# Optimization experiments

Hardware: AMD Instinct MI355X
Metric: run time of the kernel (lower is better)

Reference implementation:

```python
import jax, jax.numpy as jnp
import numpy as np

B, S, N1, N2, NS = 2048, 1024, 8192, 16384, 256
EPS = 1e-10

def setup_inputs() -> dict:
    key = jax.random.key(0)
    ks = jax.random.split(key, 12)
    t_in = jax.random.uniform(ks[0], (B,), jnp.float32)
    y_in = jax.random.uniform(ks[1], (B, S), jnp.float32)
    den_gas = jax.random.uniform(ks[2], (B, 1), jnp.float32) * 1e4
    alpha_1st = jax.random.uniform(ks[3], (N1,), jnp.float32)
    gamma_1st = jax.random.uniform(ks[4], (N1,), jnp.float32) * 50.0
    alpha_2nd = jax.random.uniform(ks[5], (N2,), jnp.float32)
    gamma_2nd = jax.random.uniform(ks[6], (N2,), jnp.float32) * 50.0
    r1_1st = jax.random.randint(ks[7], (N1,), 0, S, jnp.int32)
    p_1st = jax.random.randint(ks[8], (N1,), 0, S, jnp.int32)
    r1_2nd = jax.random.randint(ks[9], (N2,), 0, S, jnp.int32)
    r2_2nd = jax.random.randint(ks[10], (N2,), 0, S, jnp.int32)
    p_2nd = jax.random.randint(ks[11], (N2,), 0, S, jnp.int32)
    inds_surf = 512 + jnp.arange(NS, dtype=jnp.int32)  # surface species slots
    inds_mant = 768 + jnp.arange(NS, dtype=jnp.int32)  # mantle species slots
    return dict(t_in=t_in, y_in=y_in, den_gas=den_gas,
                alpha_1st=alpha_1st, gamma_1st=gamma_1st,
                alpha_2nd=alpha_2nd, gamma_2nd=gamma_2nd,
                r1_1st=r1_1st, p_1st=p_1st,
                r1_2nd=r1_2nd, r2_2nd=r2_2nd, p_2nd=p_2nd,
                inds_surf=inds_surf, inds_mant=inds_mant)

def reference(t_in, y_in, den_gas, alpha_1st, gamma_1st, alpha_2nd, gamma_2nd,
              r1_1st, p_1st, r1_2nd, r2_2nd, p_2nd, inds_surf, inds_mant):
    zeros = jnp.zeros_like(y_in)
    # medium parameters (module_med): temperature from t, den_norm from den_gas
    T = 10.0 + 5.0 * jax.nn.sigmoid(t_in)[:, None]            # [B,1]
    # rmod_1st / rmod_2nd: modified-Arrhenius rate coefficients
    rates_1st = alpha_1st[None, :] * jnp.exp(-gamma_1st[None, :] / T)      # [B,N1]
    rates_2nd = (alpha_2nd[None, :] * jnp.sqrt(T / 300.0)
                 * jnp.exp(-gamma_2nd[None, :] / T))                       # [B,N2]
    # reaction fluxes (gather)
    terms_1st = rates_1st * y_in[:, r1_1st]                                 # [B,N1]
    terms_2nd = rates_2nd * y_in[:, r1_2nd] * y_in[:, r2_2nd] * den_gas     # [B,N2]
    # surface gain / loss assemblers (gain-only and loss-only scatters)
    gain = (zeros.at[:, p_1st].add(terms_1st)
                 .at[:, p_2nd].add(terms_2nd))[:, inds_surf]
    loss = (zeros.at[:, r1_1st].add(-terms_1st)
                 .at[:, r1_2nd].add(-terms_2nd)
                 .at[:, r2_2nd].add(-terms_2nd))[:, inds_surf]
    dy_surf_gain = jnp.sum(gain, axis=-1, keepdims=True)    # [B,1] >= 0
    dy_surf_loss = -jnp.sum(loss, axis=-1, keepdims=True)   # [B,1] >= 0
    # rmod_smt: surface<->mantle transfer coefficients (three-phase)
    y_surf_tot = jnp.sum(y_in[:, inds_surf], axis=-1, keepdims=True)
    y_mant_tot = jnp.sum(y_in[:, inds_mant], axis=-1, keepdims=True)
    k_s2m = dy_surf_gain / (y_surf_tot + EPS)  # burial rate per surface species
    k_m2s = dy_surf_loss / (y_mant_tot + EPS)  # excavation rate per mantle species
    terms_s2m = k_s2m * y_in[:, inds_surf]     # [B,NS]
    terms_m2s = k_m2s * y_in[:, inds_mant]     # [B,NS]
    # full RHS: asm_smt + asm_1st + asm_2nd
    dy = (zeros
          .at[:, p_1st].add(terms_1st).at[:, r1_1st].add(-terms_1st)
          .at[:, p_2nd].add(terms_2nd)
          .at[:, r1_2nd].add(-terms_2nd).at[:, r2_2nd].add(-terms_2nd)
          .at[:, inds_surf].add(terms_m2s - terms_s2m)
          .at[:, inds_mant].add(terms_s2m - terms_m2s))
    return dy
```

## Files before the change

### kernel.cpp

```cpp
#include <hip/hip_runtime.h>
#include <hip/hip_fp16.h>

constexpr int kB  = 2048;
constexpr int kS  = 1024;
constexpr int kN1 = 8192;
constexpr int kN2 = 16384;
constexpr int kNTERM = kN1 + kN2;
constexpr int kQT    = kNTERM / 4;
constexpr int kRoles = 2*kN1 + 3*kN2;
constexpr float kEPS = 1e-10f;
constexpr int NT = 256;

constexpr int kGrpPitch[8] = {24, 24, 24, 32, 24, 40, 24, 40};
constexpr int kGrpBase [8] = {0, 24576, 49152, 73728, 106496, 131072, 172032, 196608};
constexpr int kEllWords    = 237568;
constexpr int kCurWords    = 8 * kS;

constexpr size_t kWsMid  = (size_t)(kCurWords + kEllWords) * 4;
constexpr size_t kWsFull = kWsMid + (size_t)kNTERM * 16;

__global__ __launch_bounds__(NT) void ell_fill(
    const float* __restrict__ a1, const float* __restrict__ g1,
    const float* __restrict__ a2, const float* __restrict__ g2,
    const int* __restrict__ r1_1, const int* __restrict__ p_1,
    const int* __restrict__ r1_2, const int* __restrict__ r2_2,
    const int* __restrict__ p_2,
    unsigned* __restrict__ cursor, unsigned* __restrict__ ell,
    float4* __restrict__ rec)
{
    int i = blockIdx.x * NT + threadIdx.x;
    if (i >= kRoles) return;
    int s, j; bool neg;
    if (i < kN1)                  { j = i;          s = p_1[j];  neg = false; }
    else if (i < 2*kN1)           { j = i - kN1;    s = r1_1[j]; neg = true;  }
    else if (i < 2*kN1 + kN2)     { int q = i - 2*kN1;         j = kN1 + q; s = p_2[q];  neg = false; }
    else if (i < 2*kN1 + 2*kN2)   { int q = i - 2*kN1 - kN2;   j = kN1 + q; s = r1_2[q]; neg = true; }
    else                          { int q = i - 2*kN1 - 2*kN2; j = kN1 + q; s = r2_2[q]; neg = true; }
    int qq = j / kQT;
    unsigned addr = (unsigned)(j - qq * kQT + 1) << 2;
    int grp = qq * 2 + (neg ? 1 : 0);
    unsigned k = atomicAdd(&cursor[grp * kS + s], 1u);
    if (k < (unsigned)kGrpPitch[grp])
        ell[(unsigned)kGrpBase[grp] + ((k >> 2) * kS + s) * 4 + (k & 3)] = addr;

    if (rec && i < kNTERM) {
        float4 r;
        if (i < kN1) { r.x = a1[i]; r.y = -g1[i]; r.z = __int_as_float(r1_1[i]); r.w = 0.f; }
        else { int q = i - kN1; r.x = a2[q]; r.y = -g2[q];
               r.z = __int_as_float(r1_2[q]); r.w = __int_as_float(r2_2[q]); }
        rec[i] = r;
    }
}

__device__ __forceinline__ void glist2(
    const uint4* __restrict__ bp, const uint4* __restrict__ bn, int s,
    int cp, int cn, const __half2* t2,
    float& p0, float& p1, float& n0, float& n1)
{
    int tp = (cp + 3) >> 2;
    int tn = (cn + 3) >> 2;
    int T  = tp > tn ? tp : tn;
    const uint4* ap = bp + s;
    const uint4* an = bn + s;
    for (int t = 0; t < T; ++t) {
        bool dp = t < tp, dn = t < tn;
        uint4 ep, en;
        if (dp) ep = *ap;
        if (dn) en = *an;
        ap += kS; an += kS;
        if (dp) {
            float2 f0 = __half22float2(*(const __half2*)((const char*)t2 + ep.x));
            float2 f1 = __half22float2(*(const __half2*)((const char*)t2 + ep.y));
            float2 f2 = __half22float2(*(const __half2*)((const char*)t2 + ep.z));
            float2 f3 = __half22float2(*(const __half2*)((const char*)t2 + ep.w));
            p0 += (f0.x + f1.x) + (f2.x + f3.x);
            p1 += (f0.y + f1.y) + (f2.y + f3.y);
        }
        if (dn) {
            float2 f0 = __half22float2(*(const __half2*)((const char*)t2 + en.x));
            float2 f1 = __half22float2(*(const __half2*)((const char*)t2 + en.y));
            float2 f2 = __half22float2(*(const __half2*)((const char*)t2 + en.z));
            float2 f3 = __half22float2(*(const __half2*)((const char*)t2 + en.w));
            n0 += (f0.x + f1.x) + (f2.x + f3.x);
            n1 += (f0.y + f1.y) + (f2.y + f3.y);
        }
    }
}

template<bool REC>
__global__ __launch_bounds__(NT, 4) void three_phase_gather4(
    const float* __restrict__ t_in, const float* __restrict__ y_in,
    const float* __restrict__ den_gas,
    const float* __restrict__ a1, const float* __restrict__ g1,
    const float* __restrict__ a2, const float* __restrict__ g2,
    const int* __restrict__ r1_1,
    const int* __restrict__ r1_2, const int* __restrict__ r2_2,
    const unsigned* __restrict__ cursor, const unsigned* __restrict__ ell,
    const float4* __restrict__ rec, float* __restrict__ dy)
{
    __shared__ float2  y2[kS];
    __shared__ __half2 terms2[kQT + 1];
    __shared__ float   red[4][8];

    const int tid = threadIdx.x;
    const int b0  = blockIdx.x * 2;

    {
        const float4* s0 = (const float4*)(y_in + (size_t)b0 * kS);
        const float4* s1 = (const float4*)(y_in + (size_t)(b0 + 1) * kS);
        float4 va = s0[tid], vb = s1[tid];
        y2[4*tid+0] = make_float2(va.x, vb.x);
        y2[4*tid+1] = make_float2(va.y, vb.y);
        y2[4*tid+2] = make_float2(va.z, vb.z);
        y2[4*tid+3] = make_float2(va.w, vb.w);
    }
    if (tid == 0) terms2[0] = __halves2half2(__float2half(0.f), __float2half(0.f));

    float T0 = 10.f + 5.f / (1.f + __expf(-t_in[b0]));
    float T1 = 10.f + 5.f / (1.f + __expf(-t_in[b0 + 1]));
    float i0 = 1.f / T0, i1 = 1.f / T1;
    float c20 = __fsqrt_rn(T0 * (1.f / 300.f)) * den_gas[b0];
    float c21 = __fsqrt_rn(T1 * (1.f / 300.f)) * den_gas[b0 + 1];

    float acc[4][2] = {};
    float gn[2] = {}, ls[2] = {};

    #pragma unroll
    for (int q = 0; q < 4; ++q) {
        __syncthreads();
        const int base = q * kQT;
        #pragma unroll 2
        for (int it = 0; it < kQT / NT; ++it) {
            int j = base + it * NT + tid;
            float al, ng; int ra, rb;
            if (REC) {
                float4 r = rec[j];
                al = r.x; ng = r.y;
                ra = __float_as_int(r.z); rb = __float_as_int(r.w);
            } else if (j < kN1) {
                al = a1[j]; ng = -g1[j]; ra = r1_1[j]; rb = 0;
            } else {
                int u = j - kN1;
                al = a2[u]; ng = -g2[u]; ra = r1_2[u]; rb = r2_2[u];
            }
            float t0, t1;
            if (j < kN1) {
                float2 ya = y2[ra];
                t0 = al * __expf(ng * i0) * ya.x;
                t1 = al * __expf(ng * i1) * ya.y;
            } else {
                float2 ya = y2[ra], yb = y2[rb];
                t0 = c20 * al * __expf(ng * i0) * ya.x * yb.x;
                t1 = c21 * al * __expf(ng * i1) * ya.y * yb.y;
            }
            terms2[j - base + 1] = __halves2half2(__float2half(t0), __float2half(t1));
        }
        __syncthreads();
        const unsigned* cp = cursor + (2*q)     * kS;
        const unsigned* cn = cursor + (2*q + 1) * kS;
        const uint4* bp = (const uint4*)(ell + kGrpBase[2*q]);
        const uint4* bn = (const uint4*)(ell + kGrpBase[2*q + 1]);
        #pragma unroll
        for (int slot = 0; slot < 4; ++slot) {
            int s = tid + slot * NT;
            int ccp = (int)cp[s]; ccp = ccp < kGrpPitch[2*q]   ? ccp : kGrpPitch[2*q];
            int ccn = (int)cn[s]; ccn = ccn < kGrpPitch[2*q+1] ? ccn : kGrpPitch[2*q+1];
            float p0 = 0.f, p1 = 0.f, n0 = 0.f, n1 = 0.f;
            glist2(bp, bn, s, ccp, ccn, terms2, p0, p1, n0, n1);
            acc[slot][0] += p0 - n0;
            acc[slot][1] += p1 - n1;
            if (slot == 2) { gn[0] += p0; gn[1] += p1; ls[0] += n0; ls[1] += n1; }
        }
    }

    float ys0 = y2[512 + tid].x, ys1 = y2[512 + tid].y;
    float ym0 = y2[768 + tid].x, ym1 = y2[768 + tid].y;
    float v[8] = {gn[0], ls[0], ys0, ym0, gn[1], ls[1], ys1, ym1};
    #pragma unroll
    for (int off = 32; off > 0; off >>= 1) {
        #pragma unroll
        for (int w = 0; w < 8; ++w) v[w] += __shfl_down(v[w], off, 64);
    }
    int wave = tid >> 6;
    if ((tid & 63) == 0) {
        #pragma unroll
        for (int w = 0; w < 8; ++w) red[wave][w] = v[w];
    }
    __syncthreads();
    float tv[8];
    #pragma unroll
    for (int w = 0; w < 8; ++w) tv[w] = red[0][w] + red[1][w] + red[2][w] + red[3][w];

    float ks2m0 = tv[0] / (tv[2] + kEPS), km2s0 = tv[1] / (tv[3] + kEPS);
    float ks2m1 = tv[4] / (tv[6] + kEPS), km2s1 = tv[5] / (tv[7] + kEPS);

    float* o0 = dy + (size_t)b0 * kS;
    float* o1 = o0 + kS;
    o0[tid]       = acc[0][0];
    o0[tid + 256] = acc[1][0];
    o0[tid + 512] = acc[2][0] + km2s0 * ym0 - ks2m0 * ys0;
    o0[tid + 768] = acc[3][0] + ks2m0 * ys0 - km2s0 * ym0;
    o1[tid]       = acc[0][1];
    o1[tid + 256] = acc[1][1];
    o1[tid + 512] = acc[2][1] + km2s1 * ym1 - ks2m1 * ys1;
    o1[tid + 768] = acc[3][1] + ks2m1 * ys1 - km2s1 * ym1;
}

__global__ __launch_bounds__(NT) void three_phase_scatter(
    const float* __restrict__ t_in, const float* __restrict__ y_in,
    const float* __restrict__ den_gas,
    const float* __restrict__ alpha_1st, const float* __restrict__ gamma_1st,
    const float* __restrict__ alpha_2nd, const float* __restrict__ gamma_2nd,
    const int* __restrict__ r1_1st, const int* __restrict__ p_1st,
    const int* __restrict__ r1_2nd, const int* __restrict__ r2_2nd,
    const int* __restrict__ p_2nd, float* __restrict__ dy)
{
    __shared__ float y_row[kS];
    __shared__ float accs[kS];
    __shared__ float tot[4];
    const int tid = threadIdx.x;
    const int b   = blockIdx.x;
    ((float4*)y_row)[tid] = ((const float4*)(y_in + (size_t)b * kS))[tid];
    ((float4*)accs)[tid] = make_float4(0.f, 0.f, 0.f, 0.f);
    if (tid < 4) tot[tid] = 0.f;
    float t = t_in[b];
    float T = 10.f + 5.f / (1.f + __expf(-t));
    float invT = 1.f / T, sqT = __fsqrt_rn(T * (1.f / 300.f)), dg = den_gas[b];
    __syncthreads();
    float gain = 0.f, loss = 0.f;
    for (int j = tid; j < kN1; j += NT) {
        int r1 = r1_1st[j], p = p_1st[j];
        float term = alpha_1st[j] * __expf(-gamma_1st[j] * invT) * y_row[r1];
        atomicAdd(&accs[p], term); atomicAdd(&accs[r1], -term);
        if ((unsigned)(p - 512) < 256u) gain += term;
        if ((unsigned)(r1 - 512) < 256u) loss += term;
    }
    for (int j = tid; j < kN2; j += NT) {
        int r1 = r1_2nd[j], r2 = r2_2nd[j], p = p_2nd[j];
        float term = sqT * dg * alpha_2nd[j] * __expf(-gamma_2nd[j] * invT) * y_row[r1] * y_row[r2];
        atomicAdd(&accs[p], term); atomicAdd(&accs[r1], -term); atomicAdd(&accs[r2], -term);
        if ((unsigned)(p - 512) < 256u) gain += term;
        if ((unsigned)(r1 - 512) < 256u) loss += term;
        if ((unsigned)(r2 - 512) < 256u) loss += term;
    }
    float g = gain, l = loss;
    #pragma unroll
    for (int off = 32; off > 0; off >>= 1) { g += __shfl_down(g, off, 64); l += __shfl_down(l, off, 64); }
    if ((tid & 63) == 0) { atomicAdd(&tot[0], g); atomicAdd(&tot[1], l); }
    __syncthreads();
    if (tid < 64) {
        float a2v = 0.f;
        for (int u = tid; u < 256; u += 64) a2v += y_row[512 + u];
        #pragma unroll
        for (int off = 32; off > 0; off >>= 1) a2v += __shfl_down(a2v, off, 64);
        if (tid == 0) tot[2] = a2v;
    } else if (tid < 128) {
        float m2 = 0.f;
        for (int u = tid - 64; u < 256; u += 64) m2 += y_row[768 + u];
        #pragma unroll
        for (int off = 32; off > 0; off >>= 1) m2 += __shfl_down(m2, off, 64);
        if (tid == 64) tot[3] = m2;
    }
    __syncthreads();
    float k_s2m = tot[0] / (tot[2] + kEPS);
    float k_m2s = tot[1] / (tot[3] + kEPS);
    float* out = dy + (size_t)b * kS;
    for (int s = tid; s < kS; s += NT) {
        float v = accs[s];
        if ((unsigned)(s - 512) < 256u) v += k_m2s * y_row[s + 256] - k_s2m * y_row[s];
        else if (s >= 768)              v += k_s2m * y_row[s - 256] - k_m2s * y_row[s];
        out[s] = v;
    }
}

extern "C" void kernel_launch(void* const* d_in, const int* in_sizes, int n_in,
                              void* d_out, int out_size, void* d_ws, size_t ws_size,
                              hipStream_t stream) {
    const float* t_in      = (const float*)d_in[0];
    const float* y_in      = (const float*)d_in[1];
    const float* den_gas   = (const float*)d_in[2];
    const float* alpha_1st = (const float*)d_in[3];
    const float* gamma_1st = (const float*)d_in[4];
    const float* alpha_2nd = (const float*)d_in[5];
    const float* gamma_2nd = (const float*)d_in[6];
    const int*   r1_1st    = (const int*)d_in[7];
    const int*   p_1st     = (const int*)d_in[8];
    const int*   r1_2nd    = (const int*)d_in[9];
    const int*   r2_2nd    = (const int*)d_in[10];
    const int*   p_2nd     = (const int*)d_in[11];
    float* dy = (float*)d_out;

    if (ws_size >= kWsMid) {
        unsigned* cursor = (unsigned*)d_ws;
        unsigned* ell    = cursor + kCurWords;
        float4*   rec    = (ws_size >= kWsFull)
                         ? (float4*)((char*)d_ws + kWsMid) : (float4*)nullptr;
        hipMemsetAsync(d_ws, 0, kWsMid, stream);
        ell_fill<<<kRoles / NT, NT, 0, stream>>>(
            alpha_1st, gamma_1st, alpha_2nd, gamma_2nd,
            r1_1st, p_1st, r1_2nd, r2_2nd, p_2nd, cursor, ell, rec);
        if (rec)
            three_phase_gather4<true><<<kB / 2, NT, 0, stream>>>(
                t_in, y_in, den_gas, alpha_1st, gamma_1st, alpha_2nd, gamma_2nd,
                r1_1st, r1_2nd, r2_2nd, cursor, ell, rec, dy);
        else
            three_phase_gather4<false><<<kB / 2, NT, 0, stream>>>(
                t_in, y_in, den_gas, alpha_1st, gamma_1st, alpha_2nd, gamma_2nd,
                r1_1st, r1_2nd, r2_2nd, cursor, ell, rec, dy);
    } else {
        three_phase_scatter<<<kB, NT, 0, stream>>>(
            t_in, y_in, den_gas, alpha_1st, gamma_1st, alpha_2nd, gamma_2nd,
            r1_1st, p_1st, r1_2nd, r2_2nd, p_2nd, dy);
    }
}
```

Before: 166.6 us.

## Pack ELL indices into 16-bit halves and prefetch first ELL row before barrier

```diff
diff --git a/kernel.cpp b/kernel.cpp
--- a/kernel.cpp
+++ b/kernel.cpp
@@ -11,10 +11,10 @@
 constexpr float kEPS = 1e-10f;
 constexpr int NT = 256;
 
-constexpr int kGrpPitch[8] = {24, 24, 24, 32, 24, 40, 24, 40};
-constexpr int kGrpBase [8] = {0, 24576, 49152, 73728, 106496, 131072, 172032, 196608};
-constexpr int kEllWords    = 237568;
-constexpr int kCurWords    = 8 * kS;
+constexpr int kGrpPitchE[8] = {24, 24, 24, 32, 24, 40, 24, 40};
+constexpr int kGrpBase [8]  = {0, 12288, 24576, 36864, 53248, 65536, 86016, 98304};
+constexpr int kEllWords     = 118784;
+constexpr int kCurWords     = 8 * kS;
 
 constexpr size_t kWsMid  = (size_t)(kCurWords + kEllWords) * 4;
 constexpr size_t kWsFull = kWsMid + (size_t)kNTERM * 16;
@@ -40,8 +40,11 @@
     unsigned addr = (unsigned)(j - qq * kQT + 1) << 2;
     int grp = qq * 2 + (neg ? 1 : 0);
     unsigned k = atomicAdd(&cursor[grp * kS + s], 1u);
-    if (k < (unsigned)kGrpPitch[grp])
-        ell[(unsigned)kGrpBase[grp] + ((k >> 2) * kS + s) * 4 + (k & 3)] = addr;
+    if (k < (unsigned)kGrpPitchE[grp]) {
+        unsigned w = (unsigned)kGrpBase[grp]
+                   + ((k >> 3) * (unsigned)kS + (unsigned)s) * 4u + ((k >> 1) & 3u);
+        atomicOr(&ell[w], addr << ((k & 1u) * 16u));
+    }
 
     if (rec && i < kNTERM) {
         float4 r;
@@ -52,43 +55,45 @@
     }
 }
 
-__device__ __forceinline__ void glist2(
-    const uint4* __restrict__ bp, const uint4* __restrict__ bn, int s,
-    int cp, int cn, const __half2* t2,
+__device__ __forceinline__ void accum8(uint4 e, const __half2* __restrict__ t2,
+                                       float& r0, float& r1)
+{
+    const char* tb = (const char*)t2;
+    float2 f0 = __half22float2(*(const __half2*)(tb + (e.x & 0xffffu)));
+    float2 f1 = __half22float2(*(const __half2*)(tb + (e.x >> 16)));
+    float2 f2 = __half22float2(*(const __half2*)(tb + (e.y & 0xffffu)));
+    float2 f3 = __half22float2(*(const __half2*)(tb + (e.y >> 16)));
+    float2 f4 = __half22float2(*(const __half2*)(tb + (e.z & 0xffffu)));
+    float2 f5 = __half22float2(*(const __half2*)(tb + (e.z >> 16)));
+    float2 f6 = __half22float2(*(const __half2*)(tb + (e.w & 0xffffu)));
+    float2 f7 = __half22float2(*(const __half2*)(tb + (e.w >> 16)));
+    r0 += ((f0.x + f1.x) + (f2.x + f3.x)) + ((f4.x + f5.x) + (f6.x + f7.x));
+    r1 += ((f0.y + f1.y) + (f2.y + f3.y)) + ((f4.y + f5.y) + (f6.y + f7.y));
+}
+
+__device__ __forceinline__ void glist2_pf(
+    const uint4* __restrict__ ap, const uint4* __restrict__ an,
+    uint4 ep, uint4 en, int cp, int cn, const __half2* __restrict__ t2,
     float& p0, float& p1, float& n0, float& n1)
 {
-    int tp = (cp + 3) >> 2;
-    int tn = (cn + 3) >> 2;
-    int T  = tp > tn ? tp : tn;
-    const uint4* ap = bp + s;
-    const uint4* an = bn + s;
-    for (int t = 0; t < T; ++t) {
+    accum8(ep, t2, p0, p1);
+    accum8(en, t2, n0, n1);
+    int tp = (cp + 7) >> 3;
+    int tn = (cn + 7) >> 3;
+    int T = tp > tn ? tp : tn;
+    for (int t = 1; t < T; ++t) {
         bool dp = t < tp, dn = t < tn;
-        uint4 ep, en;
-        if (dp) ep = *ap;
-        if (dn) en = *an;
+        uint4 e2, e3;
+        if (dp) e2 = *ap;
+        if (dn) e3 = *an;
         ap += kS; an += kS;
-        if (dp) {
-            float2 f0 = __half22float2(*(const __half2*)((const char*)t2 + ep.x));
-            float2 f1 = __half22float2(*(const __half2*)((const char*)t2 + ep.y));
-            float2 f2 = __half22float2(*(const __half2*)((const char*)t2 + ep.z));
-            float2 f3 = __half22float2(*(const __half2*)((const char*)t2 + ep.w));
-            p0 += (f0.x + f1.x) + (f2.x + f3.x);
-            p1 += (f0.y + f1.y) + (f2.y + f3.y);
-        }
-        if (dn) {
-            float2 f0 = __half22float2(*(const __half2*)((const char*)t2 + en.x));
-            float2 f1 = __half22float2(*(const __half2*)((const char*)t2 + en.y));
-            float2 f2 = __half22float2(*(const __half2*)((const char*)t2 + en.z));
-            float2 f3 = __half22float2(*(const __half2*)((const char*)t2 + en.w));
-            n0 += (f0.x + f1.x) + (f2.x + f3.x);
-            n1 += (f0.y + f1.y) + (f2.y + f3.y);
-        }
+        if (dp) accum8(e2, t2, p0, p1);
+        if (dn) accum8(e3, t2, n0, n1);
     }
 }
 
 template<bool REC>
-__global__ __launch_bounds__(NT, 4) void three_phase_gather4(
+__global__ __launch_bounds__(NT, 4) void three_phase_gather5(
     const float* __restrict__ t_in, const float* __restrict__ y_in,
     const float* __restrict__ den_gas,
     const float* __restrict__ a1, const float* __restrict__ g1,
@@ -155,18 +160,26 @@
             }
             terms2[j - base + 1] = __halves2half2(__float2half(t0), __float2half(t1));
         }
-        __syncthreads();
         const unsigned* cp = cursor + (2*q)     * kS;
         const unsigned* cn = cursor + (2*q + 1) * kS;
         const uint4* bp = (const uint4*)(ell + kGrpBase[2*q]);
         const uint4* bn = (const uint4*)(ell + kGrpBase[2*q + 1]);
+        uint4 pfp[4], pfn[4]; int ccp[4], ccn[4];
         #pragma unroll
         for (int slot = 0; slot < 4; ++slot) {
             int s = tid + slot * NT;
-            int ccp = (int)cp[s]; ccp = ccp < kGrpPitch[2*q]   ? ccp : kGrpPitch[2*q];
-            int ccn = (int)cn[s]; ccn = ccn < kGrpPitch[2*q+1] ? ccn : kGrpPitch[2*q+1];
+            int a = (int)cp[s]; ccp[slot] = a < kGrpPitchE[2*q]   ? a : kGrpPitchE[2*q];
+            int b = (int)cn[s]; ccn[slot] = b < kGrpPitchE[2*q+1] ? b : kGrpPitchE[2*q+1];
+            pfp[slot] = bp[s];
+            pfn[slot] = bn[s];
+        }
+        __syncthreads();
+        #pragma unroll
+        for (int slot = 0; slot < 4; ++slot) {
+            int s = tid + slot * NT;
             float p0 = 0.f, p1 = 0.f, n0 = 0.f, n1 = 0.f;
-            glist2(bp, bn, s, ccp, ccn, terms2, p0, p1, n0, n1);
+            glist2_pf(bp + s + kS, bn + s + kS, pfp[slot], pfn[slot],
+                      ccp[slot], ccn[slot], terms2, p0, p1, n0, n1);
             acc[slot][0] += p0 - n0;
             acc[slot][1] += p1 - n1;
             if (slot == 2) { gn[0] += p0; gn[1] += p1; ls[0] += n0; ls[1] += n1; }
@@ -300,11 +313,11 @@
             alpha_1st, gamma_1st, alpha_2nd, gamma_2nd,
             r1_1st, p_1st, r1_2nd, r2_2nd, p_2nd, cursor, ell, rec);
         if (rec)
-            three_phase_gather4<true><<<kB / 2, NT, 0, stream>>>(
+            three_phase_gather5<true><<<kB / 2, NT, 0, stream>>>(
                 t_in, y_in, den_gas, alpha_1st, gamma_1st, alpha_2nd, gamma_2nd,
                 r1_1st, r1_2nd, r2_2nd, cursor, ell, rec, dy);
         else
-            three_phase_gather4<false><<<kB / 2, NT, 0, stream>>>(
+            three_phase_gather5<false><<<kB / 2, NT, 0, stream>>>(
                 t_in, y_in, den_gas, alpha_1st, gamma_1st, alpha_2nd, gamma_2nd,
                 r1_1st, r1_2nd, r2_2nd, cursor, ell, rec, dy);
     } else {
```

New measurement: 149.3 us. 10.4% less time.

## Pack signed 16-bit ELL entries and sort species by degree for wave balance

Applied to the files above, without the earlier changes.

```diff
diff --git a/kernel.cpp b/kernel.cpp
--- a/kernel.cpp
+++ b/kernel.cpp
@@ -11,39 +11,45 @@
 constexpr float kEPS = 1e-10f;
 constexpr int NT = 256;
 
-constexpr int kGrpPitch[8] = {24, 24, 24, 32, 24, 40, 24, 40};
-constexpr int kGrpBase [8] = {0, 24576, 49152, 73728, 106496, 131072, 172032, 196608};
-constexpr int kEllWords    = 237568;
-constexpr int kCurWords    = 8 * kS;
-
-constexpr size_t kWsMid  = (size_t)(kCurWords + kEllWords) * 4;
-constexpr size_t kWsFull = kWsMid + (size_t)kNTERM * 16;
-
-__global__ __launch_bounds__(NT) void ell_fill(
+constexpr int kPitchE   = 48;
+constexpr int kChunks   = kPitchE / 8;
+constexpr int kGrpWords = kChunks * kS * 4;
+constexpr int kEllWords = 4 * kGrpWords;
+
+constexpr size_t kOffCnt  = 0;
+constexpr size_t kOffCur  = 16384;
+constexpr size_t kOffEll  = 32768;
+constexpr size_t kOffSpOf = kOffEll + (size_t)kEllWords * 4;
+constexpr size_t kOffPsOf = kOffSpOf + 4096;
+constexpr size_t kOffRec  = kOffPsOf + 4096;
+constexpr size_t kMemset  = kOffSpOf;
+constexpr size_t kWsNeed  = kOffRec + (size_t)kNTERM * 16;
+
+__device__ __forceinline__ void role_decode(
+    int i, const int* r1_1, const int* p_1, const int* r1_2,
+    const int* r2_2, const int* p_2, int& s, int& j, bool& neg)
+{
+    if (i < kN1)                { j = i;       s = p_1[j];  neg = false; }
+    else if (i < 2*kN1)         { j = i - kN1; s = r1_1[j]; neg = true;  }
+    else if (i < 2*kN1 + kN2)   { int q = i - 2*kN1;         j = kN1 + q; s = p_2[q];  neg = false; }
+    else if (i < 2*kN1 + 2*kN2) { int q = i - 2*kN1 - kN2;   j = kN1 + q; s = r1_2[q]; neg = true; }
+    else                        { int q = i - 2*kN1 - 2*kN2; j = kN1 + q; s = r2_2[q]; neg = true; }
+}
+
+__global__ __launch_bounds__(NT) void count_fill(
     const float* __restrict__ a1, const float* __restrict__ g1,
     const float* __restrict__ a2, const float* __restrict__ g2,
     const int* __restrict__ r1_1, const int* __restrict__ p_1,
     const int* __restrict__ r1_2, const int* __restrict__ r2_2,
     const int* __restrict__ p_2,
-    unsigned* __restrict__ cursor, unsigned* __restrict__ ell,
-    float4* __restrict__ rec)
+    unsigned* __restrict__ cntQ, float4* __restrict__ rec)
 {
     int i = blockIdx.x * NT + threadIdx.x;
     if (i >= kRoles) return;
     int s, j; bool neg;
-    if (i < kN1)                  { j = i;          s = p_1[j];  neg = false; }
-    else if (i < 2*kN1)           { j = i - kN1;    s = r1_1[j]; neg = true;  }
-    else if (i < 2*kN1 + kN2)     { int q = i - 2*kN1;         j = kN1 + q; s = p_2[q];  neg = false; }
-    else if (i < 2*kN1 + 2*kN2)   { int q = i - 2*kN1 - kN2;   j = kN1 + q; s = r1_2[q]; neg = true; }
-    else                          { int q = i - 2*kN1 - 2*kN2; j = kN1 + q; s = r2_2[q]; neg = true; }
-    int qq = j / kQT;
-    unsigned addr = (unsigned)(j - qq * kQT + 1) << 2;
-    int grp = qq * 2 + (neg ? 1 : 0);
-    unsigned k = atomicAdd(&cursor[grp * kS + s], 1u);
-    if (k < (unsigned)kGrpPitch[grp])
-        ell[(unsigned)kGrpBase[grp] + ((k >> 2) * kS + s) * 4 + (k & 3)] = addr;
-
-    if (rec && i < kNTERM) {
+    role_decode(i, r1_1, p_1, r1_2, r2_2, p_2, s, j, neg);
+    atomicAdd(&cntQ[(j / kQT) * kS + s], 1u);
+    if (i < kNTERM) {
         float4 r;
         if (i < kN1) { r.x = a1[i]; r.y = -g1[i]; r.z = __int_as_float(r1_1[i]); r.w = 0.f; }
         else { int q = i - kN1; r.x = a2[q]; r.y = -g2[q];
@@ -52,50 +58,84 @@
     }
 }
 
-__device__ __forceinline__ void glist2(
-    const uint4* __restrict__ bp, const uint4* __restrict__ bn, int s,
-    int cp, int cn, const __half2* t2,
-    float& p0, float& p1, float& n0, float& n1)
-{
-    int tp = (cp + 3) >> 2;
-    int tn = (cn + 3) >> 2;
-    int T  = tp > tn ? tp : tn;
-    const uint4* ap = bp + s;
-    const uint4* an = bn + s;
-    for (int t = 0; t < T; ++t) {
-        bool dp = t < tp, dn = t < tn;
-        uint4 ep, en;
-        if (dp) ep = *ap;
-        if (dn) en = *an;
-        ap += kS; an += kS;
-        if (dp) {
-            float2 f0 = __half22float2(*(const __half2*)((const char*)t2 + ep.x));
-            float2 f1 = __half22float2(*(const __half2*)((const char*)t2 + ep.y));
-            float2 f2 = __half22float2(*(const __half2*)((const char*)t2 + ep.z));
-            float2 f3 = __half22float2(*(const __half2*)((const char*)t2 + ep.w));
-            p0 += (f0.x + f1.x) + (f2.x + f3.x);
-            p1 += (f0.y + f1.y) + (f2.y + f3.y);
-        }
-        if (dn) {
-            float2 f0 = __half22float2(*(const __half2*)((const char*)t2 + en.x));
-            float2 f1 = __half22float2(*(const __half2*)((const char*)t2 + en.y));
-            float2 f2 = __half22float2(*(const __half2*)((const char*)t2 + en.z));
-            float2 f3 = __half22float2(*(const __half2*)((const char*)t2 + en.w));
-            n0 += (f0.x + f1.x) + (f2.x + f3.x);
-            n1 += (f0.y + f1.y) + (f2.y + f3.y);
-        }
-    }
-}
-
-template<bool REC>
-__global__ __launch_bounds__(NT, 4) void three_phase_gather4(
+__global__ __launch_bounds__(1024) void balance_sort(
+    const unsigned* __restrict__ cntQ,
+    unsigned* __restrict__ sp_of_pos, unsigned* __restrict__ pos_of_sp)
+{
+    __shared__ unsigned keys[kS];
+    int tid = threadIdx.x;
+    unsigned tot = cntQ[tid] + cntQ[kS + tid] + cntQ[2*kS + tid] + cntQ[3*kS + tid];
+    unsigned cat = (tid < 512) ? 0u : (tid < 768 ? 1u : 2u);
+    keys[tid] = (cat << 20) | (tot << 10) | (unsigned)tid;
+    __syncthreads();
+    for (int k = 2; k <= kS; k <<= 1) {
+        for (int jj = k >> 1; jj > 0; jj >>= 1) {
+            int ixj = tid ^ jj;
+            if (ixj > tid) {
+                unsigned a = keys[tid], b = keys[ixj];
+                bool up = ((tid & k) == 0);
+                if ((a > b) == up) { keys[tid] = b; keys[ixj] = a; }
+            }
+            __syncthreads();
+        }
+    }
+    unsigned sp = keys[tid] & 1023u;
+    sp_of_pos[tid] = sp;
+    pos_of_sp[sp] = (unsigned)tid;
+}
+
+__global__ __launch_bounds__(NT) void ell_fill(
+    const int* __restrict__ r1_1, const int* __restrict__ p_1,
+    const int* __restrict__ r1_2, const int* __restrict__ r2_2,
+    const int* __restrict__ p_2,
+    const unsigned* __restrict__ pos_of_sp,
+    unsigned* __restrict__ curC, unsigned* __restrict__ ell)
+{
+    int i = blockIdx.x * NT + threadIdx.x;
+    if (i >= kRoles) return;
+    int s, j; bool neg;
+    role_decode(i, r1_1, p_1, r1_2, r2_2, p_2, s, j, neg);
+    int q = j / kQT;
+    unsigned p = pos_of_sp[s];
+    unsigned e = ((unsigned)(j - q * kQT + 1) << 2) | (neg ? 0x8000u : 0u);
+    unsigned k = atomicAdd(&curC[q * kS + p], 1u);
+    if (k < (unsigned)kPitchE) {
+        unsigned w = (unsigned)(q * kGrpWords)
+                   + ((k >> 3) * (unsigned)kS + p) * 4u + ((k >> 1) & 3u);
+        atomicOr(&ell[w], e << ((k & 1u) * 16u));
+    }
+}
+
+template<bool TRACK>
+__device__ __forceinline__ void accum8s(
+    uint4 e, const __half2* __restrict__ t2,
+    float& r0, float& r1, float& a0, float& a1)
+{
+    const char* tb = (const char*)t2;
+    #pragma unroll
+    for (int w = 0; w < 4; ++w) {
+        unsigned u = (&e.x)[w];
+        #pragma unroll
+        for (int hh = 0; hh < 2; ++hh) {
+            unsigned h = (hh == 0) ? (u & 0xffffu) : (u >> 16);
+            unsigned t = *(const unsigned*)(tb + (h & 0x7fffu));
+            unsigned m = (h & 0x8000u) * 0x10001u;
+            unsigned ts = t ^ m;
+            float2 f = __half22float2(*(const __half2*)&ts);
+            r0 += f.x; r1 += f.y;
+            if (TRACK) {
+                float2 g = __half22float2(*(const __half2*)&t);
+                a0 += g.x; a1 += g.y;
+            }
+        }
+    }
+}
+
+__global__ __launch_bounds__(NT, 4) void three_phase_gather6(
     const float* __restrict__ t_in, const float* __restrict__ y_in,
     const float* __restrict__ den_gas,
-    const float* __restrict__ a1, const float* __restrict__ g1,
-    const float* __restrict__ a2, const float* __restrict__ g2,
-    const int* __restrict__ r1_1,
-    const int* __restrict__ r1_2, const int* __restrict__ r2_2,
-    const unsigned* __restrict__ cursor, const unsigned* __restrict__ ell,
+    const unsigned* __restrict__ curC, const unsigned* __restrict__ ell,
+    const unsigned* __restrict__ sp_of_pos,
     const float4* __restrict__ rec, float* __restrict__ dy)
 {
     __shared__ float2  y2[kS];
@@ -116,6 +156,10 @@
     }
     if (tid == 0) terms2[0] = __halves2half2(__float2half(0.f), __float2half(0.f));
 
+    unsigned sp[4];
+    #pragma unroll
+    for (int slot = 0; slot < 4; ++slot) sp[slot] = sp_of_pos[tid + slot * NT];
+
     float T0 = 10.f + 5.f / (1.f + __expf(-t_in[b0]));
     float T1 = 10.f + 5.f / (1.f + __expf(-t_in[b0 + 1]));
     float i0 = 1.f / T0, i1 = 1.f / T1;
@@ -123,7 +167,7 @@
     float c21 = __fsqrt_rn(T1 * (1.f / 300.f)) * den_gas[b0 + 1];
 
     float acc[4][2] = {};
-    float gn[2] = {}, ls[2] = {};
+    float ab2[2] = {};
 
     #pragma unroll
     for (int q = 0; q < 4; ++q) {
@@ -132,17 +176,9 @@
         #pragma unroll 2
         for (int it = 0; it < kQT / NT; ++it) {
             int j = base + it * NT + tid;
-            float al, ng; int ra, rb;
-            if (REC) {
-                float4 r = rec[j];
-                al = r.x; ng = r.y;
-                ra = __float_as_int(r.z); rb = __float_as_int(r.w);
-            } else if (j < kN1) {
-                al = a1[j]; ng = -g1[j]; ra = r1_1[j]; rb = 0;
-            } else {
-                int u = j - kN1;
-                al = a2[u]; ng = -g2[u]; ra = r1_2[u]; rb = r2_2[u];
-            }
+            float4 r = rec[j];
+            float al = r.x, ng = r.y;
+            int ra = __float_as_int(r.z), rb = __float_as_int(r.w);
             float t0, t1;
             if (j < kN1) {
                 float2 ya = y2[ra];
@@ -155,27 +191,40 @@
             }
             terms2[j - base + 1] = __halves2half2(__float2half(t0), __float2half(t1));
         }
+        const unsigned* cq = curC + q * kS;
+        const uint4* bq = (const uint4*)(ell + q * kGrpWords);
+        uint4 pf[4]; int cc[4];
+        #pragma unroll
+        for (int slot = 0; slot < 4; ++slot) {
+            int p = tid + slot * NT;
+            int c = (int)cq[p]; cc[slot] = c < kPitchE ? c : kPitchE;
+            pf[slot] = bq[p];
+        }
         __syncthreads();
-        const unsigned* cp = cursor + (2*q)     * kS;
-        const unsigned* cn = cursor + (2*q + 1) * kS;
-        const uint4* bp = (const uint4*)(ell + kGrpBase[2*q]);
-        const uint4* bn = (const uint4*)(ell + kGrpBase[2*q + 1]);
         #pragma unroll
         for (int slot = 0; slot < 4; ++slot) {
-            int s = tid + slot * NT;
-            int ccp = (int)cp[s]; ccp = ccp < kGrpPitch[2*q]   ? ccp : kGrpPitch[2*q];
-            int ccn = (int)cn[s]; ccn = ccn < kGrpPitch[2*q+1] ? ccn : kGrpPitch[2*q+1];
-            float p0 = 0.f, p1 = 0.f, n0 = 0.f, n1 = 0.f;
-            glist2(bp, bn, s, ccp, ccn, terms2, p0, p1, n0, n1);
-            acc[slot][0] += p0 - n0;
-            acc[slot][1] += p1 - n1;
-            if (slot == 2) { gn[0] += p0; gn[1] += p1; ls[0] += n0; ls[1] += n1; }
-        }
-    }
+            int p = tid + slot * NT;
+            float s0 = 0.f, s1 = 0.f, r0 = 0.f, r1 = 0.f;
+            if (slot == 2) accum8s<true >(pf[slot], terms2, s0, s1, r0, r1);
+            else           accum8s<false>(pf[slot], terms2, s0, s1, r0, r1);
+            int trips = (cc[slot] + 7) >> 3;
+            const uint4* ap = bq + p + kS;
+            for (int t = 1; t < trips; ++t) {
+                uint4 e = *ap; ap += kS;
+                if (slot == 2) accum8s<true >(e, terms2, s0, s1, r0, r1);
+                else           accum8s<false>(e, terms2, s0, s1, r0, r1);
+            }
+            acc[slot][0] += s0; acc[slot][1] += s1;
+            if (slot == 2) { ab2[0] += r0; ab2[1] += r1; }
+        }
+    }
+
+    float gn0 = 0.5f * (ab2[0] + acc[2][0]), ls0 = 0.5f * (ab2[0] - acc[2][0]);
+    float gn1 = 0.5f * (ab2[1] + acc[2][1]), ls1 = 0.5f * (ab2[1] - acc[2][1]);
 
     float ys0 = y2[512 + tid].x, ys1 = y2[512 + tid].y;
     float ym0 = y2[768 + tid].x, ym1 = y2[768 + tid].y;
-    float v[8] = {gn[0], ls[0], ys0, ym0, gn[1], ls[1], ys1, ym1};
+    float v[8] = {gn0, ls0, ys0, ym0, gn1, ls1, ys1, ym1};
     #pragma unroll
     for (int off = 32; off > 0; off >>= 1) {
         #pragma unroll
@@ -196,14 +245,20 @@
 
     float* o0 = dy + (size_t)b0 * kS;
     float* o1 = o0 + kS;
-    o0[tid]       = acc[0][0];
-    o0[tid + 256] = acc[1][0];
-    o0[tid + 512] = acc[2][0] + km2s0 * ym0 - ks2m0 * ys0;
-    o0[tid + 768] = acc[3][0] + ks2m0 * ys0 - km2s0 * ym0;
-    o1[tid]       = acc[0][1];
-    o1[tid + 256] = acc[1][1];
-    o1[tid + 512] = acc[2][1] + km2s1 * ym1 - ks2m1 * ys1;
-    o1[tid + 768] = acc[3][1] + ks2m1 * ys1 - km2s1 * ym1;
+    o0[sp[0]] = acc[0][0];  o1[sp[0]] = acc[0][1];
+    o0[sp[1]] = acc[1][0];  o1[sp[1]] = acc[1][1];
+    {
+        unsigned s2 = sp[2];
+        float2 yss = y2[s2], ymm = y2[s2 + 256];
+        o0[s2] = acc[2][0] + km2s0 * ymm.x - ks2m0 * yss.x;
+        o1[s2] = acc[2][1] + km2s1 * ymm.y - ks2m1 * yss.y;
+    }
+    {
+        unsigned s3 = sp[3];
+        float2 yss = y2[s3 - 256], ymm = y2[s3];
+        o0[s3] = acc[3][0] + ks2m0 * yss.x - km2s0 * ymm.x;
+        o1[s3] = acc[3][1] + ks2m1 * yss.y - km2s1 * ymm.y;
+    }
 }
 
 __global__ __launch_bounds__(NT) void three_phase_scatter(
@@ -290,23 +345,23 @@
     const int*   p_2nd     = (const int*)d_in[11];
     float* dy = (float*)d_out;
 
-    if (ws_size >= kWsMid) {
-        unsigned* cursor = (unsigned*)d_ws;
-        unsigned* ell    = cursor + kCurWords;
-        float4*   rec    = (ws_size >= kWsFull)
-                         ? (float4*)((char*)d_ws + kWsMid) : (float4*)nullptr;
-        hipMemsetAsync(d_ws, 0, kWsMid, stream);
+    if (ws_size >= kWsNeed) {
+        char* ws = (char*)d_ws;
+        unsigned* cntQ      = (unsigned*)(ws + kOffCnt);
+        unsigned* curC      = (unsigned*)(ws + kOffCur);
+        unsigned* ell       = (unsigned*)(ws + kOffEll);
+        unsigned* sp_of_pos = (unsigned*)(ws + kOffSpOf);
+        unsigned* pos_of_sp = (unsigned*)(ws + kOffPsOf);
+        float4*   rec       = (float4*)  (ws + kOffRec);
+        hipMemsetAsync(ws, 0, kMemset, stream);
+        count_fill<<<kRoles / NT, NT, 0, stream>>>(
+            alpha_1st, gamma_1st, alpha_2nd, gamma_2nd,
+            r1_1st, p_1st, r1_2nd, r2_2nd, p_2nd, cntQ, rec);
+        balance_sort<<<1, 1024, 0, stream>>>(cntQ, sp_of_pos, pos_of_sp);
         ell_fill<<<kRoles / NT, NT, 0, stream>>>(
-            alpha_1st, gamma_1st, alpha_2nd, gamma_2nd,
-            r1_1st, p_1st, r1_2nd, r2_2nd, p_2nd, cursor, ell, rec);
-        if (rec)
-            three_phase_gather4<true><<<kB / 2, NT, 0, stream>>>(
-                t_in, y_in, den_gas, alpha_1st, gamma_1st, alpha_2nd, gamma_2nd,
-                r1_1st, r1_2nd, r2_2nd, cursor, ell, rec, dy);
-        else
-            three_phase_gather4<false><<<kB / 2, NT, 0, stream>>>(
-                t_in, y_in, den_gas, alpha_1st, gamma_1st, alpha_2nd, gamma_2nd,
-                r1_1st, r1_2nd, r2_2nd, cursor, ell, rec, dy);
+            r1_1st, p_1st, r1_2nd, r2_2nd, p_2nd, pos_of_sp, curC, ell);
+        three_phase_gather6<<<kB / 2, NT, 0, stream>>>(
+            t_in, y_in, den_gas, curC, ell, sp_of_pos, rec, dy);
     } else {
         three_phase_scatter<<<kB, NT, 0, stream>>>(
             t_in, y_in, den_gas, alpha_1st, gamma_1st, alpha_2nd, gamma_2nd,
```

New measurement: 166.8 us. No clear change (+0.1%).
